# Kernel optimization log

Measured on AMD Instinct MI355X. Metric: run time of the kernel, lower is better.

Reference implementation:

```python
import jax, jax.numpy as jnp
import numpy as np

N_NODES = 100000
N_EDGES = 1600000
IN_C, HID_C, OUT_C = 128, 128, 64


def gcn_conv(x, W, b, src, dst, n_nodes):
    """PyG-style GCNConv: h = x @ W; add self-loops; symmetric deg^-1/2 norm;
    scatter-add aggregation; + bias. Self-loop contribution added analytically
    (norm for self-loop edge i->i is deg_i^-1) instead of materializing edges."""
    h = x @ W  # [N, C_out]
    # degree over dst including self-loops (edge weights are all ones)
    deg = jax.ops.segment_sum(jnp.ones((src.shape[0],), h.dtype), dst,
                              num_segments=n_nodes) + 1.0
    dinv = jax.lax.rsqrt(deg)  # deg >= 1 always
    norm = dinv[src] * dinv[dst]  # [E]
    agg = jax.ops.segment_sum(h[src] * norm[:, None], dst, num_segments=n_nodes)
    agg = agg + h * (dinv * dinv)[:, None]  # self-loop term
    return agg + b


def setup_inputs() -> dict:
    key = jax.random.key(0)
    k0, k1, k2, k3, k4, k5 = jax.random.split(key, 6)
    x = jax.random.normal(k0, (N_NODES, IN_C), dtype=jnp.float32)
    edge_index = jax.random.randint(k1, (2, N_EDGES), 0, N_NODES, dtype=jnp.int64)
    s1 = 1.0 / np.sqrt(IN_C)
    s2 = 1.0 / np.sqrt(HID_C)
    W1 = jax.random.uniform(k2, (IN_C, HID_C), jnp.float32, -s1, s1)
    b1 = jax.random.uniform(k3, (HID_C,), jnp.float32, -s1, s1)
    W2 = jax.random.uniform(k4, (HID_C, OUT_C), jnp.float32, -s2, s2)
    b2 = jax.random.uniform(k5, (OUT_C,), jnp.float32, -s2, s2)
    return {"x": x, "W1": W1, "b1": b1, "W2": W2, "b2": b2,
            "edge_index": edge_index}


def reference(x, W1, b1, W2, b2, edge_index):
    src, dst = edge_index[0], edge_index[1]
    h = gcn_conv(x, W1, b1, src, dst, N_NODES)
    h = jax.nn.relu(h)
    out = gcn_conv(h, W2, b2, src, dst, N_NODES)
    return out
```

## Files before the change

### kernel.cpp

```cpp
#include <hip/hip_runtime.h>


static constexpr int BSHIFT = 7;
static constexpr int BWIDTH = 1 << BSHIFT;
static constexpr int MAXBUCK = 2048;
static constexpr int NPART = 256;

static constexpr size_t OFF_ROW  = 458752;
static constexpr size_t OFF_CCNT = 925696;
static constexpr size_t OFF_COFF = 937984;
static constexpr size_t OFF_DINV = 962560;
static constexpr size_t OFF_CSR  = 1376256;
static constexpr size_t OFF_HS1  = 8388608;
static constexpr size_t OFF_OUT1 = 35651584;
static constexpr size_t OFF_HS2  = 62914560;
static constexpr size_t OFF_H2   = 75714560;
static constexpr size_t OFF_W1S  = 77811712;
static constexpr size_t OFF_W2S  = 77844480;

__device__ __forceinline__ unsigned short f2bf(float f) {
    unsigned u = __float_as_uint(f);
    u += 0x7fffu + ((u >> 16) & 1u);
    return (unsigned short)(u >> 16);
}

typedef __attribute__((ext_vector_type(8))) short bf16x8;
typedef __attribute__((ext_vector_type(4))) float f32x4;

__device__ __forceinline__ unsigned detect_flag(const unsigned* __restrict__ w) {
    unsigned fl = 0;
#pragma unroll
    for (int k = 1; k < 32; k += 2) fl |= w[k];
    return fl;
}

__device__ __forceinline__ int edge_dst(const unsigned* w, unsigned flag,
                                        int e, int E) {
    return flag ? (int)w[E + e] : (int)w[2 * E + 2 * e];
}
__device__ __forceinline__ int edge_src(const unsigned* w, unsigned flag,
                                        int e, int E) {
    return flag ? (int)w[e] : (int)w[2 * e];
}

__global__ __launch_bounds__(1024) void hist_wprep_kernel(
    const unsigned* __restrict__ w, unsigned* __restrict__ ccnt,
    unsigned* __restrict__ h2, int E, int nbuck,
    const float* __restrict__ W1, const float* __restrict__ W2,
    unsigned short* __restrict__ O1, unsigned short* __restrict__ O2) {
    if (blockIdx.x >= NPART) {
        const int which = blockIdx.x - NPART;
        const float* W = which ? W2 : W1;
        unsigned short* O = which ? O2 : O1;
        const int BN = which ? 64 : 128;
        const int total = 128 * BN / 4;
        for (int g = threadIdx.x; g < total; g += 1024) {
            int n = g % BN, k0 = (g / BN) * 4;
            ushort4 u;
            u.x = f2bf(W[(size_t)(k0 + 0) * BN + n]);
            u.y = f2bf(W[(size_t)(k0 + 1) * BN + n]);
            u.z = f2bf(W[(size_t)(k0 + 2) * BN + n]);
            u.w = f2bf(W[(size_t)(k0 + 3) * BN + n]);
            int off = ((((n >> 4) * 4 + (k0 >> 5)) * 16 + (n & 15)) * 4 +
                       ((k0 >> 3) & 3)) * 8 + (k0 & 4);
            *(ushort4*)(O + off) = u;
        }
        return;
    }
    __shared__ unsigned hist[MAXBUCK];
    for (int i = threadIdx.x; i < nbuck; i += 1024) hist[i] = 0;
    __syncthreads();
    const unsigned f = detect_flag(w);
    const int per = (E + NPART - 1) / NPART;
    const int e0 = blockIdx.x * per, e1 = min(E, e0 + per);
    for (int e = e0 + (int)threadIdx.x; e < e1; e += 1024)
        atomicAdd(&hist[edge_dst(w, f, e, E) >> BSHIFT], 1u);
    __syncthreads();
    for (int i = threadIdx.x; i < nbuck; i += 1024) {
        unsigned h = hist[i];
        h2[(size_t)i * NPART + blockIdx.x] = h;
        if (h) atomicAdd(&ccnt[i], h);
    }
}

__global__ __launch_bounds__(NPART) void scanoff_kernel(
    const unsigned* __restrict__ ccnt, unsigned* __restrict__ coff,
    unsigned* __restrict__ h2, int nbuck) {
    __shared__ unsigned red[NPART];
    __shared__ unsigned sh[NPART];
    const int b = blockIdx.x, t = threadIdx.x;
    unsigned p = 0;
    for (int i = t; i < b; i += NPART) p += ccnt[i];
    red[t] = p;
    __syncthreads();
#pragma unroll
    for (int off = NPART / 2; off > 0; off >>= 1) {
        if (t < off) red[t] += red[t + off];
        __syncthreads();
    }
    const unsigned coffb = red[0];
    if (t == 0) {
        coff[b] = coffb;
        if (b == nbuck - 1) coff[nbuck] = coffb + ccnt[b];
    }
    unsigned v = h2[(size_t)b * NPART + t];
    sh[t] = v;
    __syncthreads();
#pragma unroll
    for (int off = 1; off < NPART; off <<= 1) {
        unsigned a = (t >= off) ? sh[t - off] : 0u;
        __syncthreads();
        sh[t] += a;
        __syncthreads();
    }
    h2[(size_t)b * NPART + t] = coffb + sh[t] - v;
}

__global__ __launch_bounds__(1024) void partition_kernel(
    const unsigned* __restrict__ w, const unsigned* __restrict__ h2,
    unsigned* __restrict__ part, int E, int nbuck) {
    __shared__ unsigned lcur[MAXBUCK];
    for (int i = threadIdx.x; i < nbuck; i += 1024)
        lcur[i] = h2[(size_t)i * NPART + blockIdx.x];
    __syncthreads();
    const unsigned f = detect_flag(w);
    const int per = (E + NPART - 1) / NPART;
    const int e0 = blockIdx.x * per, e1 = min(E, e0 + per);
    for (int e = e0 + (int)threadIdx.x; e < e1; e += 1024) {
        int d = edge_dst(w, f, e, E);
        int s = edge_src(w, f, e, E);
        unsigned pos = atomicAdd(&lcur[d >> BSHIFT], 1u);
        part[pos] = (unsigned)s | ((unsigned)(d & (BWIDTH - 1)) << 20);
    }
}

__global__ __launch_bounds__(256) void bucket_csr_kernel(
    const unsigned* __restrict__ part, const unsigned* __restrict__ coff,
    unsigned* __restrict__ row, float* __restrict__ dinv,
    int* __restrict__ csr, int N) {
    __shared__ unsigned cnt[BWIDTH];
    __shared__ unsigned sc[BWIDTH];
    __shared__ unsigned cur[BWIDTH];
    const int b = blockIdx.x, base = b << BSHIFT, t = threadIdx.x;
    if (t < BWIDTH) cnt[t] = 0;
    __syncthreads();
    const int e0 = (int)coff[b], e1 = (int)coff[b + 1];
    for (int e = e0 + t; e < e1; e += 256)
        atomicAdd(&cnt[part[e] >> 20], 1u);
    __syncthreads();
    if (t < BWIDTH) sc[t] = cnt[t];
    __syncthreads();
#pragma unroll
    for (int off = 1; off < BWIDTH; off <<= 1) {
        unsigned a = (t < BWIDTH && t >= off) ? sc[t - off] : 0u;
        __syncthreads();
        if (t < BWIDTH) sc[t] += a;
        __syncthreads();
    }
    if (t < BWIDTH) {
        unsigned r = (unsigned)e0 + sc[t] - cnt[t];
        cur[t] = r;
        if (base + t < N) {
            row[base + t] = r;
            dinv[base + t] = rsqrtf((float)cnt[t] + 1.0f);
        }
    }
    if (t == 0 && b == (int)gridDim.x - 1) row[N] = (unsigned)e1;
    __syncthreads();
    for (int e = e0 + t; e < e1; e += 256) {
        unsigned pk = part[e];
        unsigned p = atomicAdd(&cur[pk >> 20], 1u);
        csr[p] = (int)(pk & 0xFFFFFu);
    }
}

template <int BN, bool ABF16>
__global__ __launch_bounds__(256) void gemm_mfma(
    const void* __restrict__ Av, const unsigned short* __restrict__ Bs,
    const float* __restrict__ dinv, unsigned short* __restrict__ out, int M) {
    constexpr int NT = BN / 16;
    const int t = threadIdx.x;
    const int row0 = blockIdx.x * 128;
    const int w = t >> 6, lane = t & 63;
    const int m = lane & 15, q = lane >> 4;
    const int fb = (m * 4 + q) * 8;

    const int r0 = row0 + (2 * w) * 16 + m;
    const int r1 = r0 + 16;

    f32x4 acc[2][NT];
#pragma unroll
    for (int lt = 0; lt < 2; lt++)
#pragma unroll
        for (int nt = 0; nt < NT; nt++) acc[lt][nt] = (f32x4){0.f, 0.f, 0.f, 0.f};

#pragma unroll
    for (int ks = 0; ks < 4; ks++) {
        const int k0 = ks * 32 + q * 8;
        bf16x8 a0 = (bf16x8){0, 0, 0, 0, 0, 0, 0, 0};
        bf16x8 a1 = (bf16x8){0, 0, 0, 0, 0, 0, 0, 0};
        if (ABF16) {
            const unsigned short* A = (const unsigned short*)Av;
            if (r0 < M) a0 = *(const bf16x8*)(A + (size_t)r0 * 128 + k0);
            if (r1 < M) a1 = *(const bf16x8*)(A + (size_t)r1 * 128 + k0);
        } else {
            const float* A = (const float*)Av;
            if (r0 < M) {
                const float* p = A + (size_t)r0 * 128 + k0;
                f32x4 lo = *(const f32x4*)p, hi = *(const f32x4*)(p + 4);
                a0[0] = (short)f2bf(lo[0]); a0[1] = (short)f2bf(lo[1]);
                a0[2] = (short)f2bf(lo[2]); a0[3] = (short)f2bf(lo[3]);
                a0[4] = (short)f2bf(hi[0]); a0[5] = (short)f2bf(hi[1]);
                a0[6] = (short)f2bf(hi[2]); a0[7] = (short)f2bf(hi[3]);
            }
            if (r1 < M) {
                const float* p = A + (size_t)r1 * 128 + k0;
                f32x4 lo = *(const f32x4*)p, hi = *(const f32x4*)(p + 4);
                a1[0] = (short)f2bf(lo[0]); a1[1] = (short)f2bf(lo[1]);
                a1[2] = (short)f2bf(lo[2]); a1[3] = (short)f2bf(lo[3]);
                a1[4] = (short)f2bf(hi[0]); a1[5] = (short)f2bf(hi[1]);
                a1[6] = (short)f2bf(hi[2]); a1[7] = (short)f2bf(hi[3]);
            }
        }
#pragma unroll
        for (int nt = 0; nt < NT; nt++) {
            bf16x8 b = *(const bf16x8*)(Bs + (nt * 4 + ks) * 512 + fb);
            acc[0][nt] = __builtin_amdgcn_mfma_f32_16x16x32_bf16(a0, b, acc[0][nt], 0, 0, 0);
            acc[1][nt] = __builtin_amdgcn_mfma_f32_16x16x32_bf16(a1, b, acc[1][nt], 0, 0, 0);
        }
    }

#pragma unroll
    for (int lt = 0; lt < 2; lt++) {
#pragma unroll
        for (int r = 0; r < 4; r++) {
            int row = row0 + w * 32 + lt * 16 + q * 4 + r;
            if (row < M) {
                float s = dinv[row];
#pragma unroll
                for (int nt = 0; nt < NT; nt++)
                    out[(size_t)row * BN + nt * 16 + m] = f2bf(acc[lt][nt][r] * s);
            }
        }
    }
}

template <int C, bool RELU, bool OUTBF>
__global__ __launch_bounds__(256) void agg_kernel(
    const int* __restrict__ csr, const unsigned* __restrict__ row,
    const unsigned short* __restrict__ hsb, const float* __restrict__ dinv,
    const float* __restrict__ bias, void* __restrict__ outv, int N) {
    constexpr int LPN = C / 8;
    const int tid = blockIdx.x * 256 + threadIdx.x;
    const int i = tid / LPN;
    const int l = tid % LPN;
    if (i >= N) return;

    const int co = 8 * l;
    float s0 = 0.f, s1 = 0.f, s2 = 0.f, s3 = 0.f,
          s4 = 0.f, s5 = 0.f, s6 = 0.f, s7 = 0.f;
    {
        uint4 u = *(const uint4*)(hsb + (size_t)i * C + co);
        s0 += __uint_as_float(u.x << 16); s1 += __uint_as_float(u.x & 0xffff0000u);
        s2 += __uint_as_float(u.y << 16); s3 += __uint_as_float(u.y & 0xffff0000u);
        s4 += __uint_as_float(u.z << 16); s5 += __uint_as_float(u.z & 0xffff0000u);
        s6 += __uint_as_float(u.w << 16); s7 += __uint_as_float(u.w & 0xffff0000u);
    }

    const int rs = (int)row[i], re = (int)row[i + 1];
    for (int e0 = rs; e0 < re; e0 += LPN) {
        int idx = (e0 + l < re) ? csr[e0 + l] : 0;
        const int cnt = min(LPN, re - e0);
#pragma unroll 4
        for (int j = 0; j < cnt; j++) {
            int s = __shfl(idx, j, LPN);
            uint4 u = *(const uint4*)(hsb + (size_t)s * C + co);
            s0 += __uint_as_float(u.x << 16); s1 += __uint_as_float(u.x & 0xffff0000u);
            s2 += __uint_as_float(u.y << 16); s3 += __uint_as_float(u.y & 0xffff0000u);
            s4 += __uint_as_float(u.z << 16); s5 += __uint_as_float(u.z & 0xffff0000u);
            s6 += __uint_as_float(u.w << 16); s7 += __uint_as_float(u.w & 0xffff0000u);
        }
    }

    const float sc = dinv[i];
    const float4 ba = *(const float4*)(bias + co);
    const float4 bb = *(const float4*)(bias + co + 4);
    float o0 = s0 * sc + ba.x, o1 = s1 * sc + ba.y;
    float o2 = s2 * sc + ba.z, o3 = s3 * sc + ba.w;
    float o4 = s4 * sc + bb.x, o5 = s5 * sc + bb.y;
    float o6 = s6 * sc + bb.z, o7 = s7 * sc + bb.w;
    if (RELU) {
        o0 = fmaxf(o0, 0.f); o1 = fmaxf(o1, 0.f); o2 = fmaxf(o2, 0.f);
        o3 = fmaxf(o3, 0.f); o4 = fmaxf(o4, 0.f); o5 = fmaxf(o5, 0.f);
        o6 = fmaxf(o6, 0.f); o7 = fmaxf(o7, 0.f);
    }
    if (OUTBF) {
        uint4 u;
        u.x = (unsigned)f2bf(o0) | ((unsigned)f2bf(o1) << 16);
        u.y = (unsigned)f2bf(o2) | ((unsigned)f2bf(o3) << 16);
        u.z = (unsigned)f2bf(o4) | ((unsigned)f2bf(o5) << 16);
        u.w = (unsigned)f2bf(o6) | ((unsigned)f2bf(o7) << 16);
        *(uint4*)((unsigned short*)outv + (size_t)i * C + co) = u;
    } else {
        float4 a = make_float4(o0, o1, o2, o3);
        float4 b = make_float4(o4, o5, o6, o7);
        *(float4*)((float*)outv + (size_t)i * C + co) = a;
        *(float4*)((float*)outv + (size_t)i * C + co + 4) = b;
    }
}

extern "C" void kernel_launch(void* const* d_in, const int* in_sizes, int n_in,
                              void* d_out, int out_size, void* d_ws,
                              size_t ws_size, hipStream_t stream) {
    const float* x  = (const float*)d_in[0];
    const float* W1 = (const float*)d_in[1];
    const float* b1 = (const float*)d_in[2];
    const float* W2 = (const float*)d_in[3];
    const float* b2 = (const float*)d_in[4];
    const unsigned* ew = (const unsigned*)d_in[5];
    const int E = in_sizes[5] / 2;
    const int N = in_sizes[0] / 128;
    const int nbuck = (N + BWIDTH - 1) >> BSHIFT;

    char* ws = (char*)d_ws;
    unsigned* row  = (unsigned*)(ws + OFF_ROW);
    unsigned* ccnt = (unsigned*)(ws + OFF_CCNT);
    unsigned* coff = (unsigned*)(ws + OFF_COFF);
    float* dinv    = (float*)(ws + OFF_DINV);
    int* csr       = (int*)(ws + OFF_CSR);
    unsigned short* hs1  = (unsigned short*)(ws + OFF_HS1);
    unsigned short* out1 = (unsigned short*)(ws + OFF_OUT1);
    unsigned short* hs2  = (unsigned short*)(ws + OFF_HS2);
    unsigned* h2   = (unsigned*)(ws + OFF_H2);
    unsigned short* w1s  = (unsigned short*)(ws + OFF_W1S);
    unsigned short* w2s  = (unsigned short*)(ws + OFF_W2S);
    unsigned* part = (unsigned*)(ws + OFF_HS1);

    hipMemsetAsync(ccnt, 0, (size_t)(nbuck + 1) * 4, stream);

    hist_wprep_kernel<<<NPART + 2, 1024, 0, stream>>>(ew, ccnt, h2, E, nbuck,
                                                      W1, W2, w1s, w2s);
    scanoff_kernel<<<nbuck, NPART, 0, stream>>>(ccnt, coff, h2, nbuck);
    partition_kernel<<<NPART, 1024, 0, stream>>>(ew, h2, part, E, nbuck);
    bucket_csr_kernel<<<nbuck, 256, 0, stream>>>(part, coff, row, dinv, csr, N);

    gemm_mfma<128, false><<<(N + 127) / 128, 256, 0, stream>>>(x, w1s, dinv, hs1, N);
    agg_kernel<128, true, true><<<(N * 16 + 255) / 256, 256, 0, stream>>>(
        csr, row, hs1, dinv, b1, out1, N);

    gemm_mfma<64, true><<<(N + 127) / 128, 256, 0, stream>>>(out1, w2s, dinv, hs2, N);
    agg_kernel<64, false, false><<<(N * 8 + 255) / 256, 256, 0, stream>>>(
        csr, row, hs2, dinv, b2, d_out, N);
}
```

Baseline: 278.9 us.

## Fuse bucket CSR build with first GEMM, move dinv scaling into aggregation

After: 274.4 us. About the same (-1.6%).

```diff
diff --git a/kernel.cpp b/kernel.cpp
--- a/kernel.cpp
+++ b/kernel.cpp
@@ -134,53 +134,12 @@
     }
 }
 
-__global__ __launch_bounds__(256) void bucket_csr_kernel(
-    const unsigned* __restrict__ part, const unsigned* __restrict__ coff,
-    unsigned* __restrict__ row, float* __restrict__ dinv,
-    int* __restrict__ csr, int N) {
-    __shared__ unsigned cnt[BWIDTH];
-    __shared__ unsigned sc[BWIDTH];
-    __shared__ unsigned cur[BWIDTH];
-    const int b = blockIdx.x, base = b << BSHIFT, t = threadIdx.x;
-    if (t < BWIDTH) cnt[t] = 0;
-    __syncthreads();
-    const int e0 = (int)coff[b], e1 = (int)coff[b + 1];
-    for (int e = e0 + t; e < e1; e += 256)
-        atomicAdd(&cnt[part[e] >> 20], 1u);
-    __syncthreads();
-    if (t < BWIDTH) sc[t] = cnt[t];
-    __syncthreads();
-#pragma unroll
-    for (int off = 1; off < BWIDTH; off <<= 1) {
-        unsigned a = (t < BWIDTH && t >= off) ? sc[t - off] : 0u;
-        __syncthreads();
-        if (t < BWIDTH) sc[t] += a;
-        __syncthreads();
-    }
-    if (t < BWIDTH) {
-        unsigned r = (unsigned)e0 + sc[t] - cnt[t];
-        cur[t] = r;
-        if (base + t < N) {
-            row[base + t] = r;
-            dinv[base + t] = rsqrtf((float)cnt[t] + 1.0f);
-        }
-    }
-    if (t == 0 && b == (int)gridDim.x - 1) row[N] = (unsigned)e1;
-    __syncthreads();
-    for (int e = e0 + t; e < e1; e += 256) {
-        unsigned pk = part[e];
-        unsigned p = atomicAdd(&cur[pk >> 20], 1u);
-        csr[p] = (int)(pk & 0xFFFFFu);
-    }
-}
-
-template <int BN, bool ABF16>
-__global__ __launch_bounds__(256) void gemm_mfma(
+template <int BN, bool ABF16, bool SCALE>
+__device__ __forceinline__ void gemm_body(
     const void* __restrict__ Av, const unsigned short* __restrict__ Bs,
-    const float* __restrict__ dinv, unsigned short* __restrict__ out, int M) {
+    const float* __restrict__ dinv, unsigned short* __restrict__ out,
+    int M, int row0, int t) {
     constexpr int NT = BN / 16;
-    const int t = threadIdx.x;
-    const int row0 = blockIdx.x * 128;
     const int w = t >> 6, lane = t & 63;
     const int m = lane & 15, q = lane >> 4;
     const int fb = (m * 4 + q) * 8;
@@ -236,7 +195,7 @@
         for (int r = 0; r < 4; r++) {
             int row = row0 + w * 32 + lt * 16 + q * 4 + r;
             if (row < M) {
-                float s = dinv[row];
+                float s = SCALE ? dinv[row] : 1.0f;
 #pragma unroll
                 for (int nt = 0; nt < NT; nt++)
                     out[(size_t)row * BN + nt * 16 + m] = f2bf(acc[lt][nt][r] * s);
@@ -245,7 +204,63 @@
     }
 }
 
-template <int C, bool RELU, bool OUTBF>
+template <int BN, bool ABF16>
+__global__ __launch_bounds__(256) void gemm_mfma(
+    const void* __restrict__ Av, const unsigned short* __restrict__ Bs,
+    const float* __restrict__ dinv, unsigned short* __restrict__ out, int M) {
+    gemm_body<BN, ABF16, true>(Av, Bs, dinv, out, M, blockIdx.x * 128,
+                               threadIdx.x);
+}
+
+__global__ __launch_bounds__(256, 4) void bucket_gemm_kernel(
+    const unsigned* __restrict__ part, const unsigned* __restrict__ coff,
+    unsigned* __restrict__ row, float* __restrict__ dinv,
+    int* __restrict__ csr, int N, int nbuck,
+    const float* __restrict__ x, const unsigned short* __restrict__ w1s,
+    unsigned short* __restrict__ hs1) {
+    __shared__ unsigned cnt[BWIDTH];
+    __shared__ unsigned sc[BWIDTH];
+    __shared__ unsigned cur[BWIDTH];
+    const int bid = blockIdx.x, t = threadIdx.x;
+    if (bid >= nbuck) {
+        gemm_body<128, false, false>(x, w1s, nullptr, hs1, N,
+                                     (bid - nbuck) * 128, t);
+        return;
+    }
+    const int b = bid, base = b << BSHIFT;
+    if (t < BWIDTH) cnt[t] = 0;
+    __syncthreads();
+    const int e0 = (int)coff[b], e1 = (int)coff[b + 1];
+    for (int e = e0 + t; e < e1; e += 256)
+        atomicAdd(&cnt[part[e] >> 20], 1u);
+    __syncthreads();
+    if (t < BWIDTH) sc[t] = cnt[t];
+    __syncthreads();
+#pragma unroll
+    for (int off = 1; off < BWIDTH; off <<= 1) {
+        unsigned a = (t < BWIDTH && t >= off) ? sc[t - off] : 0u;
+        __syncthreads();
+        if (t < BWIDTH) sc[t] += a;
+        __syncthreads();
+    }
+    if (t < BWIDTH) {
+        unsigned r = (unsigned)e0 + sc[t] - cnt[t];
+        cur[t] = r;
+        if (base + t < N) {
+            row[base + t] = r;
+            dinv[base + t] = rsqrtf((float)cnt[t] + 1.0f);
+        }
+    }
+    if (t == 0 && b == nbuck - 1) row[N] = (unsigned)e1;
+    __syncthreads();
+    for (int e = e0 + t; e < e1; e += 256) {
+        unsigned pk = part[e];
+        unsigned p = atomicAdd(&cur[pk >> 20], 1u);
+        csr[p] = (int)(pk & 0xFFFFFu);
+    }
+}
+
+template <int C, bool RELU, bool OUTBF, bool SCALED>
 __global__ __launch_bounds__(256) void agg_kernel(
     const int* __restrict__ csr, const unsigned* __restrict__ row,
     const unsigned short* __restrict__ hsb, const float* __restrict__ dinv,
@@ -260,11 +275,16 @@
     float s0 = 0.f, s1 = 0.f, s2 = 0.f, s3 = 0.f,
           s4 = 0.f, s5 = 0.f, s6 = 0.f, s7 = 0.f;
     {
+        const float wsf = SCALED ? 1.f : dinv[i];
         uint4 u = *(const uint4*)(hsb + (size_t)i * C + co);
-        s0 += __uint_as_float(u.x << 16); s1 += __uint_as_float(u.x & 0xffff0000u);
-        s2 += __uint_as_float(u.y << 16); s3 += __uint_as_float(u.y & 0xffff0000u);
-        s4 += __uint_as_float(u.z << 16); s5 += __uint_as_float(u.z & 0xffff0000u);
-        s6 += __uint_as_float(u.w << 16); s7 += __uint_as_float(u.w & 0xffff0000u);
+        s0 += wsf * __uint_as_float(u.x << 16);
+        s1 += wsf * __uint_as_float(u.x & 0xffff0000u);
+        s2 += wsf * __uint_as_float(u.y << 16);
+        s3 += wsf * __uint_as_float(u.y & 0xffff0000u);
+        s4 += wsf * __uint_as_float(u.z << 16);
+        s5 += wsf * __uint_as_float(u.z & 0xffff0000u);
+        s6 += wsf * __uint_as_float(u.w << 16);
+        s7 += wsf * __uint_as_float(u.w & 0xffff0000u);
     }
 
     const int rs = (int)row[i], re = (int)row[i + 1];
@@ -274,11 +294,16 @@
 #pragma unroll 4
         for (int j = 0; j < cnt; j++) {
             int s = __shfl(idx, j, LPN);
+            const float wsr = SCALED ? 1.f : dinv[s];
             uint4 u = *(const uint4*)(hsb + (size_t)s * C + co);
-            s0 += __uint_as_float(u.x << 16); s1 += __uint_as_float(u.x & 0xffff0000u);
-            s2 += __uint_as_float(u.y << 16); s3 += __uint_as_float(u.y & 0xffff0000u);
-            s4 += __uint_as_float(u.z << 16); s5 += __uint_as_float(u.z & 0xffff0000u);
-            s6 += __uint_as_float(u.w << 16); s7 += __uint_as_float(u.w & 0xffff0000u);
+            s0 += wsr * __uint_as_float(u.x << 16);
+            s1 += wsr * __uint_as_float(u.x & 0xffff0000u);
+            s2 += wsr * __uint_as_float(u.y << 16);
+            s3 += wsr * __uint_as_float(u.y & 0xffff0000u);
+            s4 += wsr * __uint_as_float(u.z << 16);
+            s5 += wsr * __uint_as_float(u.z & 0xffff0000u);
+            s6 += wsr * __uint_as_float(u.w << 16);
+            s7 += wsr * __uint_as_float(u.w & 0xffff0000u);
         }
     }
 
@@ -334,7 +359,7 @@
     unsigned* h2   = (unsigned*)(ws + OFF_H2);
     unsigned short* w1s  = (unsigned short*)(ws + OFF_W1S);
     unsigned short* w2s  = (unsigned short*)(ws + OFF_W2S);
-    unsigned* part = (unsigned*)(ws + OFF_HS1);
+    unsigned* part = (unsigned*)(ws + OFF_OUT1);
 
     hipMemsetAsync(ccnt, 0, (size_t)(nbuck + 1) * 4, stream);
 
@@ -342,13 +367,13 @@
                                                       W1, W2, w1s, w2s);
     scanoff_kernel<<<nbuck, NPART, 0, stream>>>(ccnt, coff, h2, nbuck);
     partition_kernel<<<NPART, 1024, 0, stream>>>(ew, h2, part, E, nbuck);
-    bucket_csr_kernel<<<nbuck, 256, 0, stream>>>(part, coff, row, dinv, csr, N);
-
-    gemm_mfma<128, false><<<(N + 127) / 128, 256, 0, stream>>>(x, w1s, dinv, hs1, N);
-    agg_kernel<128, true, true><<<(N * 16 + 255) / 256, 256, 0, stream>>>(
+    bucket_gemm_kernel<<<nbuck + (N + 127) / 128, 256, 0, stream>>>(
+        part, coff, row, dinv, csr, N, nbuck, x, w1s, hs1);
+
+    agg_kernel<128, true, true, false><<<(N * 16 + 255) / 256, 256, 0, stream>>>(
         csr, row, hs1, dinv, b1, out1, N);
 
     gemm_mfma<64, true><<<(N + 127) / 128, 256, 0, stream>>>(out1, w2s, dinv, hs2, N);
-    agg_kernel<64, false, false><<<(N * 8 + 255) / 256, 256, 0, stream>>>(
+    agg_kernel<64, false, false, true><<<(N * 8 + 255) / 256, 256, 0, stream>>>(
         csr, row, hs2, dinv, b2, d_out, N);
 }
```
